# Performance work log

Hardware: AMD Instinct MI355X
Metric: run time of the kernel (lower is better)

## Reference

```python
import jax, jax.numpy as jnp
import numpy as np


def setup_inputs() -> dict:
    key = jax.random.key(0)
    k1, k2, k3, k4 = jax.random.split(key, 4)
    B, n, f, k = 32768, 512, 30, 40
    X = jax.random.normal(k1, (B, n), dtype=jnp.float32)
    w1 = jax.random.normal(k2, (n, 1), dtype=jnp.float32) * 0.01
    b = jnp.zeros((1,), dtype=jnp.float32)
    v = jax.random.normal(k3, (n, f, k), dtype=jnp.float32) * 0.01
    feature2field = jax.random.randint(k4, (n,), 0, f, dtype=jnp.int32)
    return {"X": X, "w1": w1, "b": b, "v": v, "feature2field": feature2field}


def reference(X, w1, b, v, feature2field):
    # linear terms: [B]
    linear = (X @ w1).reshape(-1) + b[0]
    n = v.shape[0]
    # A[i, j] = v[i, feature2field[j]]  -> [n, n, k]
    A = v[:, feature2field, :]
    # pair coefficient C[i, j] = sum_k v[i, field[j], k] * v[j, field[i], k]
    C = jnp.einsum('ijk,jik->ij', A, A)
    # strict upper triangle matches the i<j loop in the original
    Cm = C * jnp.triu(jnp.ones((n, n), dtype=C.dtype), k=1)
    # interaction[b] = sum_{i<j} C[i,j] * X[b,i] * X[b,j]
    inter = jnp.einsum('bi,ij,bj->b', X, Cm, X)
    logits = linear + inter
    return jax.nn.sigmoid(logits)
```

## Files before the change

### kernel.cpp

```cpp
#include <hip/hip_runtime.h>
#include <hip/hip_bf16.h>
#include <math.h>


#define N_FEAT 512
#define FK 1200
#define KDIM 40
#define B_ROWS 32768
#define BM 64
#define BKS 32
#define NSTEP 16

typedef __attribute__((ext_vector_type(8))) short short8;
typedef __attribute__((ext_vector_type(16))) float f32x16;

__device__ __forceinline__ unsigned short bf16_rne(float f) {
    union { float f; unsigned int u; } c; c.f = f;
    unsigned int u = c.u;
    u += 0x7fffu + ((u >> 16) & 1u);
    return (unsigned short)(u >> 16);
}

__device__ __forceinline__ float bf16_to_f(unsigned short h) {
    union { unsigned int u; float f; } c;
    c.u = ((unsigned int)h) << 16;
    return c.f;
}

__device__ __forceinline__ void async_copy16(const void* g, void* l) {
    __builtin_amdgcn_global_load_lds(
        (const __attribute__((address_space(1))) void*)g,
        (__attribute__((address_space(3))) void*)l,
        16, 0, 0);
}

__global__ __launch_bounds__(256) void build_wpk(const float* __restrict__ v,
                                                 const int* __restrict__ f2f,
                                                 unsigned short* __restrict__ Wpk) {
    __shared__ float a_lds[FK];
    __shared__ float c_lds[256 * 44];

    const int i   = blockIdx.y;
    const int j0  = blockIdx.x * 256;
    const int tid = threadIdx.x;
    const int fi  = f2f[i];

    for (int q = tid; q < FK; q += 256) a_lds[q] = v[(size_t)i * FK + q];
    for (int q = tid; q < 2560; q += 256) {
        const int jl = q / 10, c4 = q % 10;
        *(float4*)&c_lds[jl * 44 + c4 * 4] =
            *(const float4*)&v[(size_t)(j0 + jl) * FK + fi * KDIM + c4 * 4];
    }
    __syncthreads();

    const int j  = j0 + tid;
    const int fj = f2f[j];
    const float4* a = (const float4*)&a_lds[fj * KDIM];
    const float4* c = (const float4*)&c_lds[tid * 44];
    float acc = 0.f;
#pragma unroll
    for (int q = 0; q < KDIM / 4; ++q) {
        float4 av = a[q], cv = c[q];
        acc = fmaf(av.x, cv.x, acc);
        acc = fmaf(av.y, cv.y, acc);
        acc = fmaf(av.z, cv.z, acc);
        acc = fmaf(av.w, cv.w, acc);
    }
    const unsigned short val = (i == j) ? (unsigned short)0 : bf16_rne(0.5f * acc);
    Wpk[((size_t)(j >> 3) * 512 + i) * 8 + (j & 7)] = val;
}

__global__ __launch_bounds__(512, 1) void ffm_fused(const float* __restrict__ X,
                                                    const unsigned short* __restrict__ Wpk,
                                                    const float* __restrict__ w1,
                                                    const float* __restrict__ bvec,
                                                    float* __restrict__ out) {
    __shared__ __align__(16) unsigned short As[BM * N_FEAT];
    __shared__ __align__(16) unsigned short Bs[2][N_FEAT * BKS];
    __shared__ float part[8 * BM];

    const int tid  = threadIdx.x;
    const int lane = tid & 63;
    const int wave = tid >> 6;
    const int half = lane >> 5;
    const int l31  = lane & 31;

    const size_t row0 = (size_t)blockIdx.x * BM;

    auto stage = [&](int s) {
        unsigned short* dst = (unsigned short*)Bs[s & 1];
#pragma unroll
        for (int i = 0; i < 4; ++i) {
            const int ul = i * 512 + wave * 64 + lane;
            async_copy16(Wpk + ((size_t)s * 2048 + ul) * 8, dst + (size_t)ul * 8);
        }
    };

    stage(0);
    stage(1);
    {
        const float4* X4 = (const float4*)(X + row0 * N_FEAT);
#pragma unroll
        for (int u = 0; u < 8; ++u) {
            const int g  = u * 512 + tid;
            const int r  = g >> 6;
            const int kc = g & 63;
            float4 f0 = X4[r * 128 + kc * 2];
            float4 f1 = X4[r * 128 + kc * 2 + 1];
            union { unsigned short us[8]; short8 v; } pk;
            pk.us[0] = bf16_rne(f0.x);
            pk.us[1] = bf16_rne(f0.y);
            pk.us[2] = bf16_rne(f0.z);
            pk.us[3] = bf16_rne(f0.w);
            pk.us[4] = bf16_rne(f1.x);
            pk.us[5] = bf16_rne(f1.y);
            pk.us[6] = bf16_rne(f1.z);
            pk.us[7] = bf16_rne(f1.w);
            *(short8*)(As + ((size_t)kc * 64 + (r ^ (kc & 7))) * 8) = pk.v;
        }
    }
    asm volatile("s_waitcnt lgkmcnt(0)" ::: "memory");
    __builtin_amdgcn_s_barrier();

    f32x16 acc[2][2];
#pragma unroll
    for (int mi = 0; mi < 2; ++mi)
#pragma unroll
        for (int ci = 0; ci < 2; ++ci)
#pragma unroll
            for (int r = 0; r < 16; ++r) acc[mi][ci][r] = 0.f;

    short8 fa[2][2][2], fb[2][2][2];

    asm volatile("s_waitcnt vmcnt(4)" ::: "memory");
#pragma unroll
    for (int si = 0; si < 2; ++si) {
        const int kcg = si * 2 + half;
        const int ksw = kcg & 7;
#pragma unroll
        for (int mi = 0; mi < 2; ++mi)
            fa[0][si][mi] = *(const short8*)(As + ((size_t)kcg * 64 + ((mi * 32 + l31) ^ ksw)) * 8);
#pragma unroll
        for (int ci = 0; ci < 2; ++ci)
            fb[0][si][ci] = *(const short8*)((const unsigned short*)Bs[0] +
                            ((size_t)(si * 2 + half) * 512 + wave * 64 + ci * 32 + l31) * 8);
    }

#pragma unroll
    for (int t = 0; t < NSTEP; ++t) {
        const int cur = t & 1;
        const int nxt = cur ^ 1;

        asm volatile("s_waitcnt lgkmcnt(0)" ::: "memory");
        __builtin_amdgcn_sched_barrier(0);

        if (t + 2 < NSTEP) stage(t + 2);

        if (t + 1 < NSTEP) {
            if (t + 2 < NSTEP)
                asm volatile("s_waitcnt vmcnt(4)" ::: "memory");
            else
                asm volatile("s_waitcnt vmcnt(0)" ::: "memory");
            const unsigned short* bs = (const unsigned short*)Bs[nxt];
#pragma unroll
            for (int si = 0; si < 2; ++si) {
                const int kcg = (t + 1) * 4 + si * 2 + half;
                const int ksw = kcg & 7;
#pragma unroll
                for (int mi = 0; mi < 2; ++mi)
                    fa[nxt][si][mi] = *(const short8*)(As +
                        ((size_t)kcg * 64 + ((mi * 32 + l31) ^ ksw)) * 8);
#pragma unroll
                for (int ci = 0; ci < 2; ++ci)
                    fb[nxt][si][ci] = *(const short8*)(bs +
                        ((size_t)(si * 2 + half) * 512 + wave * 64 + ci * 32 + l31) * 8);
            }
        }

        __builtin_amdgcn_s_setprio(1);
#pragma unroll
        for (int si = 0; si < 2; ++si)
#pragma unroll
            for (int mi = 0; mi < 2; ++mi)
#pragma unroll
                for (int ci = 0; ci < 2; ++ci)
                    acc[mi][ci] = __builtin_amdgcn_mfma_f32_32x32x16_bf16(
                        fa[cur][si][mi], fb[cur][si][ci], acc[mi][ci], 0, 0, 0);
        __builtin_amdgcn_s_setprio(0);
    }

    float w1v[2];
#pragma unroll
    for (int ci = 0; ci < 2; ++ci) w1v[ci] = w1[wave * 64 + ci * 32 + l31];
    const float bias = bvec[0];

    float rs[2][16];
#pragma unroll
    for (int mi = 0; mi < 2; ++mi) {
#pragma unroll
        for (int reg = 0; reg < 16; ++reg) {
            const int row = mi * 32 + (reg & 3) + 8 * (reg >> 2) + 4 * half;
            float s = 0.f;
#pragma unroll
            for (int ci = 0; ci < 2; ++ci) {
                const int gc = wave * 64 + ci * 32 + l31;
                const int kc = gc >> 3;
                const float xf = bf16_to_f(As[((size_t)kc * 64 + (row ^ (kc & 7))) * 8 + (gc & 7)]);
                s = fmaf(xf, acc[mi][ci][reg] + w1v[ci], s);
            }
            rs[mi][reg] = s;
        }
    }

#pragma unroll
    for (int mi = 0; mi < 2; ++mi)
#pragma unroll
        for (int reg = 0; reg < 16; ++reg) {
            float r = rs[mi][reg];
#pragma unroll
            for (int off = 1; off < 32; off <<= 1)
                r += __shfl_xor(r, off, 32);
            rs[mi][reg] = r;
        }
    if (l31 == 0) {
#pragma unroll
        for (int mi = 0; mi < 2; ++mi)
#pragma unroll
            for (int reg = 0; reg < 16; ++reg) {
                const int row = mi * 32 + (reg & 3) + 8 * (reg >> 2) + 4 * half;
                part[wave * 64 + row] = rs[mi][reg];
            }
    }
    __syncthreads();

    if (tid < BM) {
        float tsum = bias;
#pragma unroll
        for (int w = 0; w < 8; ++w) tsum += part[w * 64 + tid];
        out[row0 + tid] = 1.0f / (1.0f + expf(-tsum));
    }
}

extern "C" void kernel_launch(void* const* d_in, const int* in_sizes, int n_in,
                              void* d_out, int out_size, void* d_ws, size_t ws_size,
                              hipStream_t stream) {
    const float* X   = (const float*)d_in[0];
    const float* w1  = (const float*)d_in[1];
    const float* b   = (const float*)d_in[2];
    const float* v   = (const float*)d_in[3];
    const int*   f2f = (const int*)d_in[4];
    float* out = (float*)d_out;

    unsigned short* Wpk = (unsigned short*)d_ws;

    build_wpk<<<dim3(2, N_FEAT), 256, 0, stream>>>(v, f2f, Wpk);
    ffm_fused<<<B_ROWS / BM, 512, 0, stream>>>(X, Wpk, w1, b, out);
}
```

Before: 132.1 us.

## Load W fragments directly from global into registers, drop LDS staging buffer

Removes the double-buffered LDS staging of the packed pair-coefficient matrix and has each wave read its B fragments straight from global memory into registers, prefetching one step ahead. Freeing that LDS lets occupancy rise to two blocks per CU via the launch bounds. A-fragments are now loaded from LDS each step without prefetch. The cost is more global/L2 traffic per block, since each block re-reads the full W, and exposed load latency is hidden only by the register prefetch and by the extra resident block.

```diff
diff --git a/kernel.cpp b/kernel.cpp
--- a/kernel.cpp
+++ b/kernel.cpp
@@ -8,7 +8,6 @@
 #define KDIM 40
 #define B_ROWS 32768
 #define BM 64
-#define BKS 32
 #define NSTEP 16
 
 typedef __attribute__((ext_vector_type(8))) short short8;
@@ -25,13 +24,6 @@
     union { unsigned int u; float f; } c;
     c.u = ((unsigned int)h) << 16;
     return c.f;
-}
-
-__device__ __forceinline__ void async_copy16(const void* g, void* l) {
-    __builtin_amdgcn_global_load_lds(
-        (const __attribute__((address_space(1))) void*)g,
-        (__attribute__((address_space(3))) void*)l,
-        16, 0, 0);
 }
 
 __global__ __launch_bounds__(256) void build_wpk(const float* __restrict__ v,
@@ -70,13 +62,12 @@
     Wpk[((size_t)(j >> 3) * 512 + i) * 8 + (j & 7)] = val;
 }
 
-__global__ __launch_bounds__(512, 1) void ffm_fused(const float* __restrict__ X,
+__global__ __launch_bounds__(512, 2) void ffm_fused(const float* __restrict__ X,
                                                     const unsigned short* __restrict__ Wpk,
                                                     const float* __restrict__ w1,
                                                     const float* __restrict__ bvec,
                                                     float* __restrict__ out) {
     __shared__ __align__(16) unsigned short As[BM * N_FEAT];
-    __shared__ __align__(16) unsigned short Bs[2][N_FEAT * BKS];
     __shared__ float part[8 * BM];
 
     const int tid  = threadIdx.x;
@@ -87,17 +78,8 @@
 
     const size_t row0 = (size_t)blockIdx.x * BM;
 
-    auto stage = [&](int s) {
-        unsigned short* dst = (unsigned short*)Bs[s & 1];
-#pragma unroll
-        for (int i = 0; i < 4; ++i) {
-            const int ul = i * 512 + wave * 64 + lane;
-            async_copy16(Wpk + ((size_t)s * 2048 + ul) * 8, dst + (size_t)ul * 8);
-        }
-    };
-
-    stage(0);
-    stage(1);
+    const unsigned short* wp = Wpk + ((size_t)half * 512 + wave * 64 + l31) * 8;
+
     {
         const float4* X4 = (const float4*)(X + row0 * N_FEAT);
 #pragma unroll
@@ -130,51 +112,36 @@
 #pragma unroll
             for (int r = 0; r < 16; ++r) acc[mi][ci][r] = 0.f;
 
-    short8 fa[2][2][2], fb[2][2][2];
-
-    asm volatile("s_waitcnt vmcnt(4)" ::: "memory");
-#pragma unroll
-    for (int si = 0; si < 2; ++si) {
-        const int kcg = si * 2 + half;
-        const int ksw = kcg & 7;
-#pragma unroll
-        for (int mi = 0; mi < 2; ++mi)
-            fa[0][si][mi] = *(const short8*)(As + ((size_t)kcg * 64 + ((mi * 32 + l31) ^ ksw)) * 8);
+    short8 fb[2][2][2];
+#pragma unroll
+    for (int si = 0; si < 2; ++si)
 #pragma unroll
         for (int ci = 0; ci < 2; ++ci)
-            fb[0][si][ci] = *(const short8*)((const unsigned short*)Bs[0] +
-                            ((size_t)(si * 2 + half) * 512 + wave * 64 + ci * 32 + l31) * 8);
-    }
+            fb[0][si][ci] = *(const short8*)(wp + ((size_t)(si * 2) * 512 + ci * 32) * 8);
 
 #pragma unroll
     for (int t = 0; t < NSTEP; ++t) {
         const int cur = t & 1;
         const int nxt = cur ^ 1;
 
-        asm volatile("s_waitcnt lgkmcnt(0)" ::: "memory");
-        __builtin_amdgcn_sched_barrier(0);
-
-        if (t + 2 < NSTEP) stage(t + 2);
-
         if (t + 1 < NSTEP) {
-            if (t + 2 < NSTEP)
-                asm volatile("s_waitcnt vmcnt(4)" ::: "memory");
-            else
-                asm volatile("s_waitcnt vmcnt(0)" ::: "memory");
-            const unsigned short* bs = (const unsigned short*)Bs[nxt];
-#pragma unroll
-            for (int si = 0; si < 2; ++si) {
-                const int kcg = (t + 1) * 4 + si * 2 + half;
-                const int ksw = kcg & 7;
-#pragma unroll
-                for (int mi = 0; mi < 2; ++mi)
-                    fa[nxt][si][mi] = *(const short8*)(As +
-                        ((size_t)kcg * 64 + ((mi * 32 + l31) ^ ksw)) * 8);
+#pragma unroll
+            for (int si = 0; si < 2; ++si)
 #pragma unroll
                 for (int ci = 0; ci < 2; ++ci)
-                    fb[nxt][si][ci] = *(const short8*)(bs +
-                        ((size_t)(si * 2 + half) * 512 + wave * 64 + ci * 32 + l31) * 8);
-            }
+                    fb[nxt][si][ci] = *(const short8*)(wp +
+                        ((size_t)((t + 1) * 4 + si * 2) * 512 + ci * 32) * 8);
+        }
+
+        short8 a[2][2];
+#pragma unroll
+        for (int si = 0; si < 2; ++si) {
+            const int kcg = t * 4 + si * 2 + half;
+            const int ksw = kcg & 7;
+#pragma unroll
+            for (int mi = 0; mi < 2; ++mi)
+                a[si][mi] = *(const short8*)(As +
+                    ((size_t)kcg * 64 + ((mi * 32 + l31) ^ ksw)) * 8);
         }
 
         __builtin_amdgcn_s_setprio(1);
@@ -185,7 +152,7 @@
 #pragma unroll
                 for (int ci = 0; ci < 2; ++ci)
                     acc[mi][ci] = __builtin_amdgcn_mfma_f32_32x32x16_bf16(
-                        fa[cur][si][mi], fb[cur][si][ci], acc[mi][ci], 0, 0, 0);
+                        a[si][mi], fb[cur][si][ci], acc[mi][ci], 0, 0, 0);
         __builtin_amdgcn_s_setprio(0);
     }
 
```

Measured after the change: 128.2 us. 3.0% less time.
